# Performance work log

Measured on AMD Instinct MI355X. Metric: run time of the kernel, lower is better.

Reference implementation:

```python
import jax, jax.numpy as jnp
import numpy as np

# TensorProductConvLayer (DiffDock-style): gather -> edge-MLP-weighted fully
# connected tensor product (lmax=1 irreps) -> scatter-mean.
# in/out irreps: ns x0e + nv x1o + nv x1e + ns x0o ; sh irreps: 1x0e + 1x1o
NS, NV = 16, 4
N_NODES, N_EDGES = 8000, 160000
EDGE_FEAT = 3 * NS                      # 48
IRREPS_DIM = 2 * NS + 6 * NV            # 56
# per-path weight block sizes (fully-connected 'uvw' paths, mul2 = 1):
# [A:0e*0e->0e, B:1o*1o->0e, A:0e*1o->1o, B:1o*0e->1o, C:1e*1o->1o,
#  B:1o*1o->1e, C:1e*0e->1e, D:0o*1o->1e, C:1e*1o->0o, D:0o*0e->0o]
PATH_SIZES = [NS*NS, NV*NS, NS*NV, NV*NV, NV*NV, NV*NV, NV*NV, NS*NV, NV*NS, NS*NS]
W_NUMEL = sum(PATH_SIZES)               # 832
# component-normalized CG factors: 1x1->0 uses delta/sqrt(3); 1x1->1 uses eps/sqrt(2)
INV_SQRT3 = float(1.0 / np.sqrt(3.0))
INV_SQRT2 = float(1.0 / np.sqrt(2.0))
# element path normalization: 1/sqrt(total fan-in mul per output irrep)
A_SCAL = float(1.0 / np.sqrt(NS + NV))      # 0e / 0o outputs
A_VEC = float(1.0 / np.sqrt(NS + 2 * NV))   # 1o / 1e outputs


def setup_inputs() -> dict:
    key = jax.random.key(0)
    ks = jax.random.split(key, 6)
    node_attr = jax.random.normal(ks[0], (N_NODES, IRREPS_DIM), jnp.float32)
    edge_index = jax.random.randint(ks[1], (2, N_EDGES), 0, N_NODES)
    edge_attr = jax.random.normal(ks[2], (N_EDGES, EDGE_FEAT), jnp.float32)
    edge_sh = jax.random.normal(ks[3], (N_EDGES, 4), jnp.float32)
    s = float(1.0 / np.sqrt(EDGE_FEAT))
    fc_w1 = jax.random.normal(ks[4], (EDGE_FEAT, EDGE_FEAT), jnp.float32) * s
    fc_b1 = jnp.zeros((EDGE_FEAT,), jnp.float32)
    fc_w2 = jax.random.normal(ks[5], (EDGE_FEAT, W_NUMEL), jnp.float32) * s
    fc_b2 = jnp.zeros((W_NUMEL,), jnp.float32)
    return dict(node_attr=node_attr, edge_attr=edge_attr, edge_sh=edge_sh,
                fc_w1=fc_w1, fc_b1=fc_b1, fc_w2=fc_w2, fc_b2=fc_b2,
                edge_index=edge_index)


def _split_weights(w):
    outs, off = [], 0
    for sz in PATH_SIZES:
        outs.append(w[:, off:off + sz])
        off += sz
    return outs


def _tp_conv(node_attr, edge_attr, edge_sh, fc_w1, fc_b1, fc_w2, fc_b2, src, dst):
    # edge MLP -> per-edge tensor-product weights [E, 832]
    h = jax.nn.relu(edge_attr @ fc_w1 + fc_b1)
    w = h @ fc_w2 + fc_b2
    wA0, wB0, wA1, wB1, wC1, wB1e, wC1e, wD1e, wC0o, wD0o = _split_weights(w)

    x = node_attr[dst]                         # gather [E, 56]
    x0e = x[:, :NS]
    x1o = x[:, NS:NS + 3 * NV].reshape(-1, NV, 3)
    x1e = x[:, NS + 3 * NV:NS + 6 * NV].reshape(-1, NV, 3)
    x0o = x[:, NS + 6 * NV:]
    s0 = edge_sh[:, 0]
    s1 = edge_sh[:, 1:4]

    # ---- 0e output [E, ns]
    o0e = jnp.einsum('eu,euv->ev', x0e, wA0.reshape(-1, NS, NS)) * s0[:, None]
    dot_b = jnp.einsum('eui,ei->eu', x1o, s1) * INV_SQRT3   # 1o x 1o -> 0e
    o0e = (o0e + jnp.einsum('eu,euv->ev', dot_b, wB0.reshape(-1, NV, NS))) * A_SCAL

    # ---- 1o output [E, nv, 3]
    o1o = jnp.einsum('eu,euv->ev', x0e, wA1.reshape(-1, NS, NV))[:, :, None] * s1[:, None, :]
    o1o = o1o + jnp.einsum('eui,euv->evi', x1o, wB1.reshape(-1, NV, NV)) * s0[:, None, None]
    cr_e = jnp.cross(x1e, s1[:, None, :]) * INV_SQRT2       # 1e x 1o -> 1o
    o1o = (o1o + jnp.einsum('eui,euv->evi', cr_e, wC1.reshape(-1, NV, NV))) * A_VEC

    # ---- 1e output [E, nv, 3]
    cr_o = jnp.cross(x1o, s1[:, None, :]) * INV_SQRT2       # 1o x 1o -> 1e
    o1e = jnp.einsum('eui,euv->evi', cr_o, wB1e.reshape(-1, NV, NV))
    o1e = o1e + jnp.einsum('eui,euv->evi', x1e, wC1e.reshape(-1, NV, NV)) * s0[:, None, None]
    o1e = (o1e + jnp.einsum('eu,euv->ev', x0o, wD1e.reshape(-1, NS, NV))[:, :, None] * s1[:, None, :]) * A_VEC

    # ---- 0o output [E, ns]
    dot_c = jnp.einsum('eui,ei->eu', x1e, s1) * INV_SQRT3   # 1e x 1o -> 0o
    o0o = jnp.einsum('eu,euv->ev', dot_c, wC0o.reshape(-1, NV, NS))
    o0o = (o0o + jnp.einsum('eu,euv->ev', x0o, wD0o.reshape(-1, NS, NS)) * s0[:, None]) * A_SCAL

    tp = jnp.concatenate([o0e, o1o.reshape(-1, 3 * NV), o1e.reshape(-1, 3 * NV), o0o], axis=-1)

    # scatter-mean over source nodes
    summed = jax.ops.segment_sum(tp, src, num_segments=N_NODES)
    counts = jax.ops.segment_sum(jnp.ones((tp.shape[0],), tp.dtype), src, num_segments=N_NODES)
    return summed / jnp.maximum(counts, 1.0)[:, None]


def reference(node_attr, edge_attr, edge_sh, fc_w1, fc_b1, fc_w2, fc_b2, edge_index):
    src, dst = edge_index[0], edge_index[1]
    return _tp_conv(node_attr, edge_attr, edge_sh, fc_w1, fc_b1, fc_w2, fc_b2, src, dst)
```

## Files before the change

kernel.cpp:

```cpp
#include <hip/hip_runtime.h>
#include <hip/hip_fp16.h>

#define IRR    56
#define EF     48
#define WN     832
#define NEDGE  160000
#define NNODE  8000
#define NT     256
#define TE2    64
#define NTASK  (NEDGE / TE2)
#define GRID   (2 * NTASK)

#define INV_SQRT3 0.5773502691896258f
#define INV_SQRT2 0.7071067811865476f
#define A_SCAL    0.22360679774997896f
#define A_VEC     0.20412414523193154f

typedef __bf16 bf16x8 __attribute__((ext_vector_type(8)));
typedef float  f32x4  __attribute__((ext_vector_type(4)));
typedef unsigned short u16x8 __attribute__((ext_vector_type(8)));
typedef unsigned short u16x4 __attribute__((ext_vector_type(4)));

__device__ __forceinline__ unsigned short f2bf(float f) {
    unsigned int u = __builtin_bit_cast(unsigned int, f);
    u += 0x7FFFu + ((u >> 16) & 1u);
    return (unsigned short)(u >> 16);
}

__global__ void k_setup(const float* __restrict__ w1, const float* __restrict__ b1,
                        const float* __restrict__ w2, const float* __restrict__ b2,
                        unsigned short* __restrict__ W1T, unsigned short* __restrict__ W2L,
                        const int* __restrict__ edge_index, int* __restrict__ hist)
{
    int o = blockIdx.x * 256 + threadIdx.x;
    if (o < 52 * 2 * 64 * 8) {
        int i = o >> 10;
        int rem = o & 1023;
        int f = rem >> 9;
        int rem2 = rem & 511;
        int l = rem2 >> 3, j = rem2 & 7;
        int mm = l & 15, qq = l >> 4;
        int k = f * 32 + qq * 8 + j;
        int n = i * 16 + mm;
        float v = (k < EF) ? w2[k * WN + n] : ((k == EF) ? b2[n] : 0.f);
        W2L[o] = f2bf(v);
    }
    if (o < EF * EF) { int k = o / EF, n = o - k * EF; W1T[n * 64 + k] = f2bf(w1[o]); }
    if (o < EF * 16) { int n = o >> 4, kk = EF + (o & 15); W1T[n * 64 + kk] = (kk == EF) ? f2bf(b1[n]) : (unsigned short)0; }
    if (o < NEDGE) atomicAdd(&hist[edge_index[o]], 1);
}

__global__ __launch_bounds__(NT, 4) void tp_fused(
    const float* __restrict__ node_attr,
    const float* __restrict__ edge_attr,
    const float* __restrict__ edge_sh,
    const int*   __restrict__ edge_index,
    const int*   __restrict__ hist,
    const unsigned short* __restrict__ W1T,
    const unsigned short* __restrict__ W2L,
    float* __restrict__ out)
{
    __shared__ __align__(16) unsigned char UGH[TE2 * 56 * 4];
    __shared__ __align__(16) float sF[TE2 * 61];
    __shared__ __align__(16) float sO[TE2 * 28];
    __shared__ int   sSrc[TE2], sDst[TE2];
    __shared__ float sInv[TE2];

    float*          sG = (float*)UGH;
    unsigned short* sH = (unsigned short*)UGH;

    const int tid    = threadIdx.x;
    const int lane   = tid & 63;
    const int wv     = tid >> 6;
    const int m      = lane & 15;
    const int quad   = lane >> 4;
    const int em     = wv * 16 + m;
    const int flavor = blockIdx.x & 1;
    const int e0     = (blockIdx.x >> 1) * TE2;

    if (tid < TE2)            sSrc[tid]       = edge_index[e0 + tid];
    else if (tid < 2 * TE2)   sDst[tid - TE2] = edge_index[NEDGE + e0 + tid - TE2];
    __syncthreads();

    {
        const float* nrow = node_attr + (size_t)sDst[em] * IRR;
        float* g = sG + em * 56;
        #pragma unroll
        for (int t = 0; t < 3; t++) {
            int c = quad + t * 4;
            *(float4*)(g + c * 4) = *(const float4*)(nrow + c * 4);
        }
        if (quad < 2) { int c = 12 + quad; *(float4*)(g + c * 4) = *(const float4*)(nrow + c * 4); }
    }
    if (tid >= 128 && tid < 128 + TE2) {
        int e = tid - 128;
        sInv[e] = 1.0f / fmaxf((float)hist[sSrc[e]], 1.0f);
    }

    float4 sh4 = *(const float4*)&edge_sh[(size_t)(e0 + em) * 4];
    const float s0 = sh4.x, sx = sh4.y, sy = sh4.z, sz = sh4.w;

    {
        const float* x = sG + em * 56;
        float* F = sF + em * 61;
        const float c0S = s0 * A_SCAL;
        const float c0V = s0 * A_VEC;
        const float cD3 = INV_SQRT3 * A_SCAL;
        const float cC2 = INV_SQRT2 * A_VEC;
        if (flavor == 0) {
            #pragma unroll
            for (int t = 0; t < 4; t++) {
                int u = quad * 4 + t;
                float x0e = x[u];
                F[u]      = x0e * c0S;
                F[20 + u] = x0e * A_VEC;
            }
            {
                int u = quad;
                float a0 = x[16 + u*3], a1 = x[16 + u*3 + 1], a2 = x[16 + u*3 + 2];
                float b0 = x[28 + u*3], b1 = x[28 + u*3 + 1], b2 = x[28 + u*3 + 2];
                F[16 + u] = (a0*sx + a1*sy + a2*sz) * cD3;
                F[36 + u*3 + 0] = a0 * c0V;
                F[36 + u*3 + 1] = a1 * c0V;
                F[36 + u*3 + 2] = a2 * c0V;
                F[48 + u*3 + 0] = (b1*sz - b2*sy) * cC2;
                F[48 + u*3 + 1] = (b2*sx - b0*sz) * cC2;
                F[48 + u*3 + 2] = (b0*sy - b1*sx) * cC2;
            }
        } else {
            {
                int u = quad;
                float a0 = x[16 + u*3], a1 = x[16 + u*3 + 1], a2 = x[16 + u*3 + 2];
                float b0 = x[28 + u*3], b1 = x[28 + u*3 + 1], b2 = x[28 + u*3 + 2];
                F[u*3 + 0]      = (a1*sz - a2*sy) * cC2;
                F[u*3 + 1]      = (a2*sx - a0*sz) * cC2;
                F[u*3 + 2]      = (a0*sy - a1*sx) * cC2;
                F[12 + u*3 + 0] = b0 * c0V;
                F[12 + u*3 + 1] = b1 * c0V;
                F[12 + u*3 + 2] = b2 * c0V;
                F[40 + u]       = (b0*sx + b1*sy + b2*sz) * cD3;
            }
            #pragma unroll
            for (int t = 0; t < 4; t++) {
                int u = quad * 4 + t;
                float x0o = x[40 + u];
                F[24 + u] = x0o * A_VEC;
                F[44 + u] = x0o * c0S;
            }
        }
    }

    bf16x8 hb0, hb1;
    {
        const float* arow = edge_attr + (size_t)(e0 + em) * EF;
        float av0[8], av1[8];
        {
            float4 p0 = *(const float4*)(arow + quad * 8);
            float4 p1 = *(const float4*)(arow + quad * 8 + 4);
            av0[0]=p0.x; av0[1]=p0.y; av0[2]=p0.z; av0[3]=p0.w;
            av0[4]=p1.x; av0[5]=p1.y; av0[6]=p1.z; av0[7]=p1.w;
        }
        if (quad < 2) {
            float4 p0 = *(const float4*)(arow + 32 + quad * 8);
            float4 p1 = *(const float4*)(arow + 32 + quad * 8 + 4);
            av1[0]=p0.x; av1[1]=p0.y; av1[2]=p0.z; av1[3]=p0.w;
            av1[4]=p1.x; av1[5]=p1.y; av1[6]=p1.z; av1[7]=p1.w;
        } else {
            #pragma unroll
            for (int j = 0; j < 8; j++) av1[j] = 0.f;
            if (quad == 2) av1[0] = 1.f;
        }
        u16x8 ub0, ub1;
        #pragma unroll
        for (int j = 0; j < 8; j++) { ub0[j] = f2bf(av0[j]); ub1[j] = f2bf(av1[j]); }
        hb0 = __builtin_bit_cast(bf16x8, ub0);
        hb1 = __builtin_bit_cast(bf16x8, ub1);
    }

    __syncthreads();

    #pragma unroll
    for (int nth = 0; nth < 3; nth++) {
        bf16x8 a0 = __builtin_bit_cast(bf16x8, *(const u16x8*)&W1T[(nth*16 + m)*64 + quad*8]);
        bf16x8 a1 = __builtin_bit_cast(bf16x8, *(const u16x8*)&W1T[(nth*16 + m)*64 + 32 + quad*8]);
        f32x4 c = {0.f, 0.f, 0.f, 0.f};
        c = __builtin_amdgcn_mfma_f32_16x16x32_bf16(a0, hb0, c, 0, 0, 0);
        c = __builtin_amdgcn_mfma_f32_16x16x32_bf16(a1, hb1, c, 0, 0, 0);
        u16x4 hp;
        #pragma unroll
        for (int r = 0; r < 4; r++) hp[r] = f2bf(fmaxf(c[r], 0.f));
        *(u16x4*)&sH[em * 72 + nth*16 + quad*4] = hp;
    }
    if (quad == 3) {
        u16x4 b = {0x3F80, 0, 0, 0}, z = {0, 0, 0, 0};
        *(u16x4*)&sH[em * 72 + 48] = b;
        *(u16x4*)&sH[em * 72 + 52] = z;
        *(u16x4*)&sH[em * 72 + 56] = z;
        *(u16x4*)&sH[em * 72 + 60] = z;
    }

    bf16x8 HB0 = __builtin_bit_cast(bf16x8, *(const u16x8*)&sH[em * 72 + quad*8]);
    bf16x8 HB1 = __builtin_bit_cast(bf16x8, *(const u16x8*)&sH[em * 72 + 32 + quad*8]);

    const float* Fp = sF + em * 61;
    const unsigned short* Wt = W2L + (size_t)flavor * 26 * 1024;

    if (flavor == 0) {
        float oe[4] = {0.f,0.f,0.f,0.f};
        float sA[4] = {0.f,0.f,0.f,0.f};
        float t1[12] = {0.f,0.f,0.f,0.f,0.f,0.f,0.f,0.f,0.f,0.f,0.f,0.f};
        #pragma unroll
        for (int i = 0; i < 26; i++) {
            u16x8 Af = *(const u16x8*)&Wt[i * 1024 + lane * 8];
            u16x8 Bf = *(const u16x8*)&Wt[i * 1024 + 512 + lane * 8];
            f32x4 c = {0.f,0.f,0.f,0.f};
            c = __builtin_amdgcn_mfma_f32_16x16x32_bf16(__builtin_bit_cast(bf16x8, Af), HB0, c, 0, 0, 0);
            c = __builtin_amdgcn_mfma_f32_16x16x32_bf16(__builtin_bit_cast(bf16x8, Bf), HB1, c, 0, 0, 0);
            if (i < 20) {
                float f = Fp[i];
                #pragma unroll
                for (int r = 0; r < 4; r++) oe[r] += f * c[r];
            } else if (i < 24) {
                float f = Fp[20 + (i - 20)*4 + quad];
                #pragma unroll
                for (int r = 0; r < 4; r++) sA[r] += f * c[r];
            } else {
                int u = (i - 24)*4 + quad;
                #pragma unroll
                for (int i3 = 0; i3 < 3; i3++) {
                    float f = Fp[36 + u*3 + i3];
                    #pragma unroll
                    for (int r = 0; r < 4; r++) t1[i3*4 + r] += f * c[r];
                }
            }
        }
        #pragma unroll
        for (int r = 0; r < 4; r++) {
            sA[r] += __shfl_xor(sA[r], 16, 64);  sA[r] += __shfl_xor(sA[r], 32, 64);
        }
        #pragma unroll
        for (int i = 0; i < 12; i++) {
            t1[i] += __shfl_xor(t1[i], 16, 64);  t1[i] += __shfl_xor(t1[i], 32, 64);
        }
        float4 v0; v0.x = oe[0]; v0.y = oe[1]; v0.z = oe[2]; v0.w = oe[3];
        *(float4*)&sO[em * 28 + quad*4] = v0;
        if (quad == 0) {
            #pragma unroll
            for (int r = 0; r < 4; r++) {
                sO[em * 28 + 16 + r*3 + 0] = sA[r] * sx + t1[0*4 + r];
                sO[em * 28 + 16 + r*3 + 1] = sA[r] * sy + t1[1*4 + r];
                sO[em * 28 + 16 + r*3 + 2] = sA[r] * sz + t1[2*4 + r];
            }
        }
    } else {
        float sD[4] = {0.f,0.f,0.f,0.f};
        float t1[12] = {0.f,0.f,0.f,0.f,0.f,0.f,0.f,0.f,0.f,0.f,0.f,0.f};
        float oo[4] = {0.f,0.f,0.f,0.f};
        #pragma unroll
        for (int i = 0; i < 26; i++) {
            u16x8 Af = *(const u16x8*)&Wt[i * 1024 + lane * 8];
            u16x8 Bf = *(const u16x8*)&Wt[i * 1024 + 512 + lane * 8];
            f32x4 c = {0.f,0.f,0.f,0.f};
            c = __builtin_amdgcn_mfma_f32_16x16x32_bf16(__builtin_bit_cast(bf16x8, Af), HB0, c, 0, 0, 0);
            c = __builtin_amdgcn_mfma_f32_16x16x32_bf16(__builtin_bit_cast(bf16x8, Bf), HB1, c, 0, 0, 0);
            if (i < 2) {
                int j = i*4 + quad;
                #pragma unroll
                for (int i3 = 0; i3 < 3; i3++) {
                    float f = Fp[j*3 + i3];
                    #pragma unroll
                    for (int r = 0; r < 4; r++) t1[i3*4 + r] += f * c[r];
                }
            } else if (i < 6) {
                float f = Fp[24 + (i - 2)*4 + quad];
                #pragma unroll
                for (int r = 0; r < 4; r++) sD[r] += f * c[r];
            } else {
                float f = Fp[40 + (i - 6)];
                #pragma unroll
                for (int r = 0; r < 4; r++) oo[r] += f * c[r];
            }
        }
        #pragma unroll
        for (int r = 0; r < 4; r++) {
            sD[r] += __shfl_xor(sD[r], 16, 64);  sD[r] += __shfl_xor(sD[r], 32, 64);
        }
        #pragma unroll
        for (int i = 0; i < 12; i++) {
            t1[i] += __shfl_xor(t1[i], 16, 64);  t1[i] += __shfl_xor(t1[i], 32, 64);
        }
        float4 v1; v1.x = oo[0]; v1.y = oo[1]; v1.z = oo[2]; v1.w = oo[3];
        *(float4*)&sO[em * 28 + 12 + quad*4] = v1;
        if (quad == 0) {
            #pragma unroll
            for (int r = 0; r < 4; r++) {
                sO[em * 28 + r*3 + 0] = sD[r] * sx + t1[0*4 + r];
                sO[em * 28 + r*3 + 1] = sD[r] * sy + t1[1*4 + r];
                sO[em * 28 + r*3 + 2] = sD[r] * sz + t1[2*4 + r];
            }
        }
    }

    __syncthreads();

    #pragma unroll
    for (int it = 0; it < 7; it++) {
        int idx = it * NT + tid;
        int e = idx / 28, ch = idx - e * 28;
        unsafeAtomicAdd(&out[(size_t)sSrc[e] * IRR + flavor * 28 + ch],
                        sO[e * 28 + ch] * sInv[e]);
    }
}

extern "C" void kernel_launch(void* const* d_in, const int* in_sizes, int n_in,
                              void* d_out, int out_size, void* d_ws, size_t ws_size,
                              hipStream_t stream) {
    const float* node_attr  = (const float*)d_in[0];
    const float* edge_attr  = (const float*)d_in[1];
    const float* edge_sh    = (const float*)d_in[2];
    const float* fc_w1      = (const float*)d_in[3];
    const float* fc_b1      = (const float*)d_in[4];
    const float* fc_w2      = (const float*)d_in[5];
    const float* fc_b2      = (const float*)d_in[6];
    const int*   edge_index = (const int*)d_in[7];

    int* hist = (int*)d_ws;
    unsigned short* W1T = (unsigned short*)(hist + NNODE);
    unsigned short* W2L = W1T + EF * 64;

    hipMemsetAsync(hist, 0, NNODE * sizeof(int), stream);
    hipMemsetAsync(d_out, 0, (size_t)out_size * sizeof(float), stream);

    k_setup<<<(NEDGE + 255) / 256, 256, 0, stream>>>(
        fc_w1, fc_b1, fc_w2, fc_b2, W1T, W2L, edge_index, hist);

    tp_fused<<<GRID, NT, 0, stream>>>(node_attr, edge_attr, edge_sh, edge_index,
                                      hist, W1T, W2L, (float*)d_out);
}
```

Baseline: 176.8 us.

## Replace atomic scatter-mean with CSR slot writes and per-node segmented reduce

Builds a CSR ordering of edges by source node (histogram, single-block scan, atomic slot assignment). The main kernel then writes each edge's tensor-product result to its sorted slot instead of issuing float atomics into the output. A separate reduce kernel sums each node's contiguous rows and divides by the count. The aim is to remove atomic contention on the output. In exchange it adds three extra launches, a large intermediate buffer of about 36 MB, and a serial single-block scan. It falls back to the old atomic path when the workspace is too small.

```diff
diff --git a/kernel.cpp b/kernel.cpp
--- a/kernel.cpp
+++ b/kernel.cpp
@@ -50,6 +50,62 @@
     if (o < NEDGE) atomicAdd(&hist[edge_index[o]], 1);
 }
 
+__global__ __launch_bounds__(256) void k_scan(const int* __restrict__ hist, int* __restrict__ offs)
+{
+    __shared__ int part[256];
+    int t = threadIdx.x;
+    int s = 0;
+    #pragma unroll
+    for (int j = 0; j < 32; j++) { int i = t * 32 + j; s += (i < NNODE) ? hist[i] : 0; }
+    part[t] = s;
+    __syncthreads();
+    for (int d = 1; d < 256; d <<= 1) {
+        int v = (t >= d) ? part[t - d] : 0;
+        __syncthreads();
+        part[t] += v;
+        __syncthreads();
+    }
+    int run = (t > 0) ? part[t - 1] : 0;
+    #pragma unroll
+    for (int j = 0; j < 32; j++) {
+        int i = t * 32 + j;
+        if (i < NNODE) { offs[i] = run; run += hist[i]; }
+    }
+}
+
+__global__ __launch_bounds__(256) void k_slot(const int* __restrict__ edge_index,
+                                              const int* __restrict__ offs,
+                                              int* __restrict__ cursor,
+                                              int* __restrict__ slot)
+{
+    int e = blockIdx.x * 256 + threadIdx.x;
+    if (e < NEDGE) {
+        int s = edge_index[e];
+        slot[e] = offs[s] + atomicAdd(&cursor[s], 1);
+    }
+}
+
+__global__ __launch_bounds__(256) void k_reduce(const float* __restrict__ tpbuf,
+                                                const int* __restrict__ offs,
+                                                const int* __restrict__ hist,
+                                                float* __restrict__ out)
+{
+    int node = blockIdx.x * 4 + (threadIdx.x >> 6);
+    int lane = threadIdx.x & 63;
+    if (node >= NNODE || lane >= IRR) return;
+    int base = offs[node], cnt = hist[node];
+    const float* p = tpbuf + (size_t)base * IRR + lane;
+    float a0 = 0.f, a1 = 0.f, a2 = 0.f, a3 = 0.f;
+    int r = 0;
+    for (; r + 4 <= cnt; r += 4) {
+        a0 += p[0]; a1 += p[IRR]; a2 += p[2 * IRR]; a3 += p[3 * IRR];
+        p += 4 * IRR;
+    }
+    for (; r < cnt; ++r) { a0 += p[0]; p += IRR; }
+    float s = (a0 + a1) + (a2 + a3);
+    out[(size_t)node * IRR + lane] = s / fmaxf((float)cnt, 1.0f);
+}
+
 __global__ __launch_bounds__(NT, 4) void tp_fused(
     const float* __restrict__ node_attr,
     const float* __restrict__ edge_attr,
@@ -58,12 +114,14 @@
     const int*   __restrict__ hist,
     const unsigned short* __restrict__ W1T,
     const unsigned short* __restrict__ W2L,
+    const int*   __restrict__ slot,
+    float* __restrict__ tpbuf,
     float* __restrict__ out)
 {
     __shared__ __align__(16) unsigned char UGH[TE2 * 56 * 4];
     __shared__ __align__(16) float sF[TE2 * 61];
     __shared__ __align__(16) float sO[TE2 * 28];
-    __shared__ int   sSrc[TE2], sDst[TE2];
+    __shared__ int   sSrc[TE2], sDst[TE2], sSlot[TE2];
     __shared__ float sInv[TE2];
 
     float*          sG = (float*)UGH;
@@ -77,9 +135,11 @@
     const int em     = wv * 16 + m;
     const int flavor = blockIdx.x & 1;
     const int e0     = (blockIdx.x >> 1) * TE2;
-
-    if (tid < TE2)            sSrc[tid]       = edge_index[e0 + tid];
-    else if (tid < 2 * TE2)   sDst[tid - TE2] = edge_index[NEDGE + e0 + tid - TE2];
+    const bool csr   = (tpbuf != nullptr);
+
+    if (tid < TE2)                 sSrc[tid]        = edge_index[e0 + tid];
+    else if (tid < 2 * TE2)        sDst[tid - TE2]  = edge_index[NEDGE + e0 + tid - TE2];
+    else if (csr && tid < 3 * TE2) sSlot[tid - 2 * TE2] = slot[e0 + tid - 2 * TE2];
     __syncthreads();
 
     {
@@ -92,7 +152,7 @@
         }
         if (quad < 2) { int c = 12 + quad; *(float4*)(g + c * 4) = *(const float4*)(nrow + c * 4); }
     }
-    if (tid >= 128 && tid < 128 + TE2) {
+    if (!csr && tid >= 128 && tid < 128 + TE2) {
         int e = tid - 128;
         sInv[e] = 1.0f / fmaxf((float)hist[sSrc[e]], 1.0f);
     }
@@ -303,12 +363,21 @@
 
     __syncthreads();
 
-    #pragma unroll
-    for (int it = 0; it < 7; it++) {
-        int idx = it * NT + tid;
-        int e = idx / 28, ch = idx - e * 28;
-        unsafeAtomicAdd(&out[(size_t)sSrc[e] * IRR + flavor * 28 + ch],
-                        sO[e * 28 + ch] * sInv[e]);
+    if (csr) {
+        #pragma unroll
+        for (int it = 0; it < 7; it++) {
+            int idx = it * NT + tid;
+            int e = idx / 28, ch = idx - e * 28;
+            tpbuf[(size_t)sSlot[e] * IRR + flavor * 28 + ch] = sO[e * 28 + ch];
+        }
+    } else {
+        #pragma unroll
+        for (int it = 0; it < 7; it++) {
+            int idx = it * NT + tid;
+            int e = idx / 28, ch = idx - e * 28;
+            unsafeAtomicAdd(&out[(size_t)sSrc[e] * IRR + flavor * 28 + ch],
+                            sO[e * 28 + ch] * sInv[e]);
+        }
     }
 }
 
@@ -324,16 +393,32 @@
     const float* fc_b2      = (const float*)d_in[6];
     const int*   edge_index = (const int*)d_in[7];
 
-    int* hist = (int*)d_ws;
-    unsigned short* W1T = (unsigned short*)(hist + NNODE);
+    int* hist   = (int*)d_ws;
+    int* cursor = hist + NNODE;
+    int* offs   = cursor + NNODE;
+    unsigned short* W1T = (unsigned short*)(offs + NNODE);
     unsigned short* W2L = W1T + EF * 64;
-
-    hipMemsetAsync(hist, 0, NNODE * sizeof(int), stream);
-    hipMemsetAsync(d_out, 0, (size_t)out_size * sizeof(float), stream);
-
-    k_setup<<<(NEDGE + 255) / 256, 256, 0, stream>>>(
-        fc_w1, fc_b1, fc_w2, fc_b2, W1T, W2L, edge_index, hist);
-
-    tp_fused<<<GRID, NT, 0, stream>>>(node_attr, edge_attr, edge_sh, edge_index,
-                                      hist, W1T, W2L, (float*)d_out);
-}
+    int*   slot  = (int*)(W2L + 52 * 2 * 64 * 8);
+    float* tpbuf = (float*)(slot + NEDGE);
+
+    size_t need = (size_t)((char*)(tpbuf + (size_t)NEDGE * IRR) - (char*)d_ws);
+    bool csr = (ws_size >= need);
+
+    if (csr) {
+        hipMemsetAsync(hist, 0, 2 * NNODE * sizeof(int), stream);
+        k_setup<<<(NEDGE + 255) / 256, 256, 0, stream>>>(
+            fc_w1, fc_b1, fc_w2, fc_b2, W1T, W2L, edge_index, hist);
+        k_scan<<<1, 256, 0, stream>>>(hist, offs);
+        k_slot<<<(NEDGE + 255) / 256, 256, 0, stream>>>(edge_index, offs, cursor, slot);
+        tp_fused<<<GRID, NT, 0, stream>>>(node_attr, edge_attr, edge_sh, edge_index,
+                                          hist, W1T, W2L, slot, tpbuf, (float*)d_out);
+        k_reduce<<<(NNODE + 3) / 4, 256, 0, stream>>>(tpbuf, offs, hist, (float*)d_out);
+    } else {
+        hipMemsetAsync(hist, 0, NNODE * sizeof(int), stream);
+        hipMemsetAsync(d_out, 0, (size_t)out_size * sizeof(float), stream);
+        k_setup<<<(NEDGE + 255) / 256, 256, 0, stream>>>(
+            fc_w1, fc_b1, fc_w2, fc_b2, W1T, W2L, edge_index, hist);
+        tp_fused<<<GRID, NT, 0, stream>>>(node_attr, edge_attr, edge_sh, edge_index,
+                                          hist, W1T, W2L, nullptr, nullptr, (float*)d_out);
+    }
+}
```

New measurement: 198.3 us. 1.12x slower.

## Merge both output flavors into one 512-thread block sharing gather and edge MLP

Applied to the files above, without the earlier changes.

Each block now holds 512 threads: four waves compute the even-parity outputs and four compute the odd-parity outputs for the same 64 edges. The node gather, edge_sh load and first MLP layer are done once per edge tile instead of twice. The W2 layout setup is reindexed to a coalesced-read form. Costs are an extra barrier, half of the threads idling during the hidden-layer MFMA, and larger shared-memory use per block, which may reduce occupancy.

```diff
diff --git a/kernel.cpp b/kernel.cpp
--- a/kernel.cpp
+++ b/kernel.cpp
@@ -6,10 +6,10 @@
 #define WN     832
 #define NEDGE  160000
 #define NNODE  8000
-#define NT     256
+#define NT     512
 #define TE2    64
 #define NTASK  (NEDGE / TE2)
-#define GRID   (2 * NTASK)
+#define GRID   NTASK
 
 #define INV_SQRT3 0.5773502691896258f
 #define INV_SQRT2 0.7071067811865476f
@@ -33,17 +33,14 @@
                         const int* __restrict__ edge_index, int* __restrict__ hist)
 {
     int o = blockIdx.x * 256 + threadIdx.x;
-    if (o < 52 * 2 * 64 * 8) {
-        int i = o >> 10;
-        int rem = o & 1023;
-        int f = rem >> 9;
-        int rem2 = rem & 511;
-        int l = rem2 >> 3, j = rem2 & 7;
-        int mm = l & 15, qq = l >> 4;
-        int k = f * 32 + qq * 8 + j;
-        int n = i * 16 + mm;
+    if (o < 64 * 832) {
+        int k = o / 832;
+        int n = o - k * 832;
         float v = (k < EF) ? w2[k * WN + n] : ((k == EF) ? b2[n] : 0.f);
-        W2L[o] = f2bf(v);
+        int i = n >> 4, mm = n & 15;
+        int f = k >> 5, q = (k >> 3) & 3, j = k & 7;
+        int o2 = (((i * 2 + f) * 64) + (q * 16 + mm)) * 8 + j;
+        W2L[o2] = f2bf(v);
     }
     if (o < EF * EF) { int k = o / EF, n = o - k * EF; W1T[n * 64 + k] = f2bf(w1[o]); }
     if (o < EF * 16) { int n = o >> 4, kk = EF + (o & 15); W1T[n * 64 + kk] = (kk == EF) ? f2bf(b1[n]) : (unsigned short)0; }
@@ -61,53 +58,58 @@
     float* __restrict__ out)
 {
     __shared__ __align__(16) unsigned char UGH[TE2 * 56 * 4];
-    __shared__ __align__(16) float sF[TE2 * 61];
-    __shared__ __align__(16) float sO[TE2 * 28];
+    __shared__ __align__(16) float sF0[TE2 * 61];
+    __shared__ __align__(16) float sF1[TE2 * 61];
+    __shared__ __align__(16) float sO[TE2 * IRR];
     __shared__ int   sSrc[TE2], sDst[TE2];
     __shared__ float sInv[TE2];
 
     float*          sG = (float*)UGH;
     unsigned short* sH = (unsigned short*)UGH;
 
-    const int tid    = threadIdx.x;
-    const int lane   = tid & 63;
-    const int wv     = tid >> 6;
-    const int m      = lane & 15;
-    const int quad   = lane >> 4;
-    const int em     = wv * 16 + m;
-    const int flavor = blockIdx.x & 1;
-    const int e0     = (blockIdx.x >> 1) * TE2;
-
-    if (tid < TE2)            sSrc[tid]       = edge_index[e0 + tid];
-    else if (tid < 2 * TE2)   sDst[tid - TE2] = edge_index[NEDGE + e0 + tid - TE2];
+    const int tid   = threadIdx.x;
+    const int lane  = tid & 63;
+    const int wv    = tid >> 6;
+    const int half  = wv >> 2;
+    const int wl    = wv & 3;
+    const int m     = lane & 15;
+    const int quad  = lane >> 4;
+    const int em    = wl * 16 + m;
+    const int e0    = blockIdx.x * TE2;
+
+    if (tid < TE2)          sSrc[tid]       = edge_index[e0 + tid];
+    else if (tid < 2 * TE2) sDst[tid - TE2] = edge_index[NEDGE + e0 + tid - TE2];
     __syncthreads();
 
     {
         const float* nrow = node_attr + (size_t)sDst[em] * IRR;
         float* g = sG + em * 56;
-        #pragma unroll
-        for (int t = 0; t < 3; t++) {
-            int c = quad + t * 4;
-            *(float4*)(g + c * 4) = *(const float4*)(nrow + c * 4);
-        }
-        if (quad < 2) { int c = 12 + quad; *(float4*)(g + c * 4) = *(const float4*)(nrow + c * 4); }
-    }
-    if (tid >= 128 && tid < 128 + TE2) {
-        int e = tid - 128;
+        if (half == 0) {
+            *(float4*)(g + quad * 4)        = *(const float4*)(nrow + quad * 4);
+            *(float4*)(g + (quad + 4) * 4)  = *(const float4*)(nrow + (quad + 4) * 4);
+        } else {
+            *(float4*)(g + (quad + 8) * 4)  = *(const float4*)(nrow + (quad + 8) * 4);
+            if (quad < 2) { int c = 12 + quad; *(float4*)(g + c * 4) = *(const float4*)(nrow + c * 4); }
+        }
+    }
+    if (tid >= 256 && tid < 256 + TE2) {
+        int e = tid - 256;
         sInv[e] = 1.0f / fmaxf((float)hist[sSrc[e]], 1.0f);
     }
 
     float4 sh4 = *(const float4*)&edge_sh[(size_t)(e0 + em) * 4];
     const float s0 = sh4.x, sx = sh4.y, sy = sh4.z, sz = sh4.w;
 
+    __syncthreads();
+
     {
         const float* x = sG + em * 56;
-        float* F = sF + em * 61;
         const float c0S = s0 * A_SCAL;
         const float c0V = s0 * A_VEC;
         const float cD3 = INV_SQRT3 * A_SCAL;
         const float cC2 = INV_SQRT2 * A_VEC;
-        if (flavor == 0) {
+        if (half == 0) {
+            float* F = sF0 + em * 61;
             #pragma unroll
             for (int t = 0; t < 4; t++) {
                 int u = quad * 4 + t;
@@ -128,6 +130,7 @@
                 F[48 + u*3 + 2] = (b0*sy - b1*sx) * cC2;
             }
         } else {
+            float* F = sF1 + em * 61;
             {
                 int u = quad;
                 float a0 = x[16 + u*3], a1 = x[16 + u*3 + 1], a2 = x[16 + u*3 + 2];
@@ -151,7 +154,7 @@
     }
 
     bf16x8 hb0, hb1;
-    {
+    if (half == 0) {
         const float* arow = edge_attr + (size_t)(e0 + em) * EF;
         float av0[8], av1[8];
         {
@@ -179,33 +182,36 @@
 
     __syncthreads();
 
-    #pragma unroll
-    for (int nth = 0; nth < 3; nth++) {
-        bf16x8 a0 = __builtin_bit_cast(bf16x8, *(const u16x8*)&W1T[(nth*16 + m)*64 + quad*8]);
-        bf16x8 a1 = __builtin_bit_cast(bf16x8, *(const u16x8*)&W1T[(nth*16 + m)*64 + 32 + quad*8]);
-        f32x4 c = {0.f, 0.f, 0.f, 0.f};
-        c = __builtin_amdgcn_mfma_f32_16x16x32_bf16(a0, hb0, c, 0, 0, 0);
-        c = __builtin_amdgcn_mfma_f32_16x16x32_bf16(a1, hb1, c, 0, 0, 0);
-        u16x4 hp;
-        #pragma unroll
-        for (int r = 0; r < 4; r++) hp[r] = f2bf(fmaxf(c[r], 0.f));
-        *(u16x4*)&sH[em * 72 + nth*16 + quad*4] = hp;
-    }
-    if (quad == 3) {
-        u16x4 b = {0x3F80, 0, 0, 0}, z = {0, 0, 0, 0};
-        *(u16x4*)&sH[em * 72 + 48] = b;
-        *(u16x4*)&sH[em * 72 + 52] = z;
-        *(u16x4*)&sH[em * 72 + 56] = z;
-        *(u16x4*)&sH[em * 72 + 60] = z;
-    }
+    if (half == 0) {
+        #pragma unroll
+        for (int nth = 0; nth < 3; nth++) {
+            bf16x8 a0 = __builtin_bit_cast(bf16x8, *(const u16x8*)&W1T[(nth*16 + m)*64 + quad*8]);
+            bf16x8 a1 = __builtin_bit_cast(bf16x8, *(const u16x8*)&W1T[(nth*16 + m)*64 + 32 + quad*8]);
+            f32x4 c = {0.f, 0.f, 0.f, 0.f};
+            c = __builtin_amdgcn_mfma_f32_16x16x32_bf16(a0, hb0, c, 0, 0, 0);
+            c = __builtin_amdgcn_mfma_f32_16x16x32_bf16(a1, hb1, c, 0, 0, 0);
+            u16x4 hp;
+            #pragma unroll
+            for (int r = 0; r < 4; r++) hp[r] = f2bf(fmaxf(c[r], 0.f));
+            *(u16x4*)&sH[em * 72 + nth*16 + quad*4] = hp;
+        }
+        if (quad == 3) {
+            u16x4 b = {0x3F80, 0, 0, 0}, z = {0, 0, 0, 0};
+            *(u16x4*)&sH[em * 72 + 48] = b;
+            *(u16x4*)&sH[em * 72 + 52] = z;
+            *(u16x4*)&sH[em * 72 + 56] = z;
+            *(u16x4*)&sH[em * 72 + 60] = z;
+        }
+    }
+    __syncthreads();
 
     bf16x8 HB0 = __builtin_bit_cast(bf16x8, *(const u16x8*)&sH[em * 72 + quad*8]);
     bf16x8 HB1 = __builtin_bit_cast(bf16x8, *(const u16x8*)&sH[em * 72 + 32 + quad*8]);
 
-    const float* Fp = sF + em * 61;
-    const unsigned short* Wt = W2L + (size_t)flavor * 26 * 1024;
-
-    if (flavor == 0) {
+    const unsigned short* Wt = W2L + (size_t)half * 26 * 1024;
+
+    if (half == 0) {
+        const float* Fp = sF0 + em * 61;
         float oe[4] = {0.f,0.f,0.f,0.f};
         float sA[4] = {0.f,0.f,0.f,0.f};
         float t1[12] = {0.f,0.f,0.f,0.f,0.f,0.f,0.f,0.f,0.f,0.f,0.f,0.f};
@@ -243,16 +249,17 @@
             t1[i] += __shfl_xor(t1[i], 16, 64);  t1[i] += __shfl_xor(t1[i], 32, 64);
         }
         float4 v0; v0.x = oe[0]; v0.y = oe[1]; v0.z = oe[2]; v0.w = oe[3];
-        *(float4*)&sO[em * 28 + quad*4] = v0;
+        *(float4*)&sO[em * IRR + quad*4] = v0;
         if (quad == 0) {
             #pragma unroll
             for (int r = 0; r < 4; r++) {
-                sO[em * 28 + 16 + r*3 + 0] = sA[r] * sx + t1[0*4 + r];
-                sO[em * 28 + 16 + r*3 + 1] = sA[r] * sy + t1[1*4 + r];
-                sO[em * 28 + 16 + r*3 + 2] = sA[r] * sz + t1[2*4 + r];
+                sO[em * IRR + 16 + r*3 + 0] = sA[r] * sx + t1[0*4 + r];
+                sO[em * IRR + 16 + r*3 + 1] = sA[r] * sy + t1[1*4 + r];
+                sO[em * IRR + 16 + r*3 + 2] = sA[r] * sz + t1[2*4 + r];
             }
         }
     } else {
+        const float* Fp = sF1 + em * 61;
         float sD[4] = {0.f,0.f,0.f,0.f};
         float t1[12] = {0.f,0.f,0.f,0.f,0.f,0.f,0.f,0.f,0.f,0.f,0.f,0.f};
         float oo[4] = {0.f,0.f,0.f,0.f};
@@ -290,13 +297,13 @@
             t1[i] += __shfl_xor(t1[i], 16, 64);  t1[i] += __shfl_xor(t1[i], 32, 64);
         }
         float4 v1; v1.x = oo[0]; v1.y = oo[1]; v1.z = oo[2]; v1.w = oo[3];
-        *(float4*)&sO[em * 28 + 12 + quad*4] = v1;
+        *(float4*)&sO[em * IRR + 28 + 12 + quad*4] = v1;
         if (quad == 0) {
             #pragma unroll
             for (int r = 0; r < 4; r++) {
-                sO[em * 28 + r*3 + 0] = sD[r] * sx + t1[0*4 + r];
-                sO[em * 28 + r*3 + 1] = sD[r] * sy + t1[1*4 + r];
-                sO[em * 28 + r*3 + 2] = sD[r] * sz + t1[2*4 + r];
+                sO[em * IRR + 28 + r*3 + 0] = sD[r] * sx + t1[0*4 + r];
+                sO[em * IRR + 28 + r*3 + 1] = sD[r] * sy + t1[1*4 + r];
+                sO[em * IRR + 28 + r*3 + 2] = sD[r] * sz + t1[2*4 + r];
             }
         }
     }
@@ -306,9 +313,8 @@
     #pragma unroll
     for (int it = 0; it < 7; it++) {
         int idx = it * NT + tid;
-        int e = idx / 28, ch = idx - e * 28;
-        unsafeAtomicAdd(&out[(size_t)sSrc[e] * IRR + flavor * 28 + ch],
-                        sO[e * 28 + ch] * sInv[e]);
+        int e = idx / IRR, ch = idx - e * IRR;
+        unsafeAtomicAdd(&out[(size_t)sSrc[e] * IRR + ch], sO[e * IRR + ch] * sInv[e]);
     }
 }
 
```

New measurement: 168.7 us. 1.05x faster.
